# Optimization experiments

Measured on AMD Instinct MI355X. Metric: run time of the kernel, lower is better.

## Reference

```python
import jax, jax.numpy as jnp
import numpy as np

N_NODES = 50000
N_EDGES = 600000  # incidence entries; hyperedge ids also live in [0, N_NODES)
HID = 128


def _prelu(x, a):
    return jnp.where(x >= 0, x, a * x)


def _hypergraph_conv(x, W, b, node_idx, edge_idx, num_nodes, num_hedges):
    # PyG HypergraphConv (use_attention=False, heads=1):
    # out = D^{-1} H B^{-1} H^T (X Theta) + bias
    xw = x @ W  # [N, F]
    ones = jnp.ones(node_idx.shape[0], dtype=x.dtype)
    D = jax.ops.segment_sum(ones, node_idx, num_segments=num_nodes)   # node degree
    B = jax.ops.segment_sum(ones, edge_idx, num_segments=num_hedges)  # hyperedge degree
    Dinv = jnp.where(D > 0, 1.0 / D, 0.0)
    Binv = jnp.where(B > 0, 1.0 / B, 0.0)
    # node -> hyperedge aggregation, scaled by B^{-1}
    m = jax.ops.segment_sum(xw[node_idx], edge_idx, num_segments=num_hedges) * Binv[:, None]
    # hyperedge -> node aggregation, scaled by D^{-1}
    out = jax.ops.segment_sum(m[edge_idx], node_idx, num_segments=num_nodes) * Dinv[:, None]
    return out + b


def setup_inputs() -> dict:
    key = jax.random.key(0)
    k1, k2, k3, k4, k5 = jax.random.split(key, 5)
    x = jax.random.normal(k1, (N_NODES, HID), dtype=jnp.float32)
    hyper_edge_index = jax.random.randint(k2, (2, N_EDGES), 0, N_NODES, dtype=jnp.int64)
    # kaiming-normal-ish linear weights, zero biases (per init_weights)
    std = float(np.sqrt(2.0 / HID))
    W1 = jax.random.normal(k3, (HID, HID), dtype=jnp.float32) * std
    W2 = jax.random.normal(k4, (HID, HID), dtype=jnp.float32) * std
    b1 = jnp.zeros((HID,), dtype=jnp.float32)
    b2 = jnp.zeros((HID,), dtype=jnp.float32)
    prelu_a = jnp.full((1,), 0.25, dtype=jnp.float32)  # nn.PReLU default
    return {"x": x, "hyper_edge_index": hyper_edge_index,
            "W1": W1, "b1": b1, "W2": W2, "b2": b2, "prelu_a": prelu_a}


def reference(x, hyper_edge_index, W1, b1, W2, b2, prelu_a):
    node_idx = hyper_edge_index[0]
    edge_idx = hyper_edge_index[1]
    h = _hypergraph_conv(x, W1, b1, node_idx, edge_idx, N_NODES, N_NODES)
    h = _prelu(h, prelu_a)
    h = _hypergraph_conv(h, W2, b2, node_idx, edge_idx, N_NODES, N_NODES)
    h = h + x  # residual
    return _prelu(h, prelu_a)
```

## Files before the change

kernel.cpp:

```cpp
#include <hip/hip_runtime.h>

typedef unsigned short u16;
typedef unsigned int   u32;
typedef unsigned long long u64;

#define HID 128
#define KPB 256
#define NBMAX 512
#define IPB 2048
#define CAP 6144
#define LSTRIDE 136

typedef __bf16 bf16x8 __attribute__((ext_vector_type(8)));
typedef float  f32x4  __attribute__((ext_vector_type(4)));

__device__ inline float u2f(u32 u){ union{u32 u;float f;} v; v.u=u; return v.f; }
__device__ inline u32   f2u(float f){ union{float f;u32 u;} v; v.f=f; return v.u; }
__device__ inline u32  f2bfu(float f){ u32 b=f2u(f); return ((b + 0x7FFFu + ((b>>16)&1u))>>16)&0xFFFFu; }
__device__ inline float blo(u32 u){ return u2f(u<<16); }
__device__ inline float bhi(u32 u){ return u2f(u & 0xFFFF0000u); }
__device__ inline u32  pk(float lo, float hi){ return (f2bfu(hi)<<16) | f2bfu(lo); }

__global__ __launch_bounds__(256) void k_hist_wfrag(const int* __restrict__ nidx, const int* __restrict__ eidx,
                                                    int* __restrict__ hist, int nE, int nN, int nb, int nhb,
                                                    const float* __restrict__ W1, const float* __restrict__ W2,
                                                    u16* __restrict__ W1f, u16* __restrict__ W2f){
    __shared__ int h[NBMAX];
    if ((int)blockIdx.x < nhb){
        for (int t=threadIdx.x; t<nb; t+=256) h[t]=0;
        __syncthreads();
        int base = blockIdx.x*IPB;
        for (int k=threadIdx.x; k<IPB; k+=256){
            int j = base+k;
            if (j < nE){
                atomicAdd(&h[nidx[j]>>8], 1);
                atomicAdd(&h[(nN+eidx[j])>>8], 1);
            }
        }
        __syncthreads();
        for (int t=threadIdx.x; t<nb; t+=256) if (h[t]) atomicAdd(&hist[t], h[t]);
    } else {
        int gid = ((int)blockIdx.x - nhb)*256 + threadIdx.x;
        const float* W = (gid < 16384) ? W1 : W2;
        u16* Wf = (gid < 16384) ? W1f : W2f;
        int id = gid & 16383;
        int i = id & 7, l = (id>>3)&63, j = (id>>9)&7, s = id>>12;
        Wf[id] = (u16)f2bfu(W[(s*32 + ((l>>4)<<3) + i)*HID + (j<<4) + (l&15)]);
    }
}

__global__ __launch_bounds__(256) void k_part_gemm(const int* __restrict__ nidx, const int* __restrict__ eidx,
                                                   const int* __restrict__ hist, int* __restrict__ bfill,
                                                   u64* __restrict__ pairs, int nE, int nN, int nb, int npb,
                                                   const float* __restrict__ A, const u16* __restrict__ Wf,
                                                   u16* __restrict__ C, int M){
    __shared__ int h[NBMAX], rsv[NBMAX], fl[NBMAX], bb[NBMAX], sd[256];
    int t = threadIdx.x;
    if ((int)blockIdx.x < npb){
        for (int i=t; i<nb; i+=256){ h[i]=0; fl[i]=0; }
        __syncthreads();
        int base = blockIdx.x*IPB;
        for (int k=t; k<IPB; k+=256){
            int j = base+k;
            if (j < nE){
                atomicAdd(&h[nidx[j]>>8], 1);
                atomicAdd(&h[(nN+eidx[j])>>8], 1);
            }
        }
        int c0 = (2*t   < nb) ? hist[2*t]   : 0;
        int c1 = (2*t+1 < nb) ? hist[2*t+1] : 0;
        int s = c0 + c1;
        sd[t] = s; __syncthreads();
        for (int o=1;o<256;o<<=1){ int u = (t>=o)? sd[t-o] : 0; __syncthreads(); sd[t]+=u; __syncthreads(); }
        int ex = sd[t] - s;
        if (2*t   < nb) bb[2*t]   = ex;
        if (2*t+1 < nb) bb[2*t+1] = ex + c0;
        __syncthreads();
        for (int i=t; i<nb; i+=256){ if (h[i]) rsv[i] = bb[i] + atomicAdd(&bfill[i], h[i]); }
        __syncthreads();
        for (int k=t; k<IPB; k+=256){
            int j = base+k;
            if (j < nE){
                int n = nidx[j], e = eidx[j];
                int b1 = n>>8;
                int p1 = rsv[b1] + atomicAdd(&fl[b1], 1);
                pairs[p1] = ((u64)(u32)n << 32) | (u32)e;
                int k2 = nN + e;
                int b2 = k2>>8;
                int p2 = rsv[b2] + atomicAdd(&fl[b2], 1);
                pairs[p2] = ((u64)(u32)k2 << 32) | (u32)n;
            }
        }
    } else {
        int wave = ((int)blockIdx.x - npb)*4 + (t>>6);
        int lane = t & 63;
        int rtiles = M >> 4;
        if (wave >= rtiles) return;
        int row0 = wave << 4;
        const float* Arow = A + (size_t)(row0 + (lane&15))*HID + ((lane>>4)<<3);
        const bf16x8* Wp = reinterpret_cast<const bf16x8*>(Wf) + lane;
        f32x4 acc[8];
        #pragma unroll
        for (int j=0;j<8;++j) acc[j] = (f32x4){0.f,0.f,0.f,0.f};
        #pragma unroll
        for (int s=0;s<4;++s){
            float4 f0 = *reinterpret_cast<const float4*>(Arow + s*32);
            float4 f1 = *reinterpret_cast<const float4*>(Arow + s*32 + 4);
            union { u16 h[8]; bf16x8 v; } au;
            au.h[0]=(u16)f2bfu(f0.x); au.h[1]=(u16)f2bfu(f0.y); au.h[2]=(u16)f2bfu(f0.z); au.h[3]=(u16)f2bfu(f0.w);
            au.h[4]=(u16)f2bfu(f1.x); au.h[5]=(u16)f2bfu(f1.y); au.h[6]=(u16)f2bfu(f1.z); au.h[7]=(u16)f2bfu(f1.w);
            #pragma unroll
            for (int j=0;j<8;++j){
                bf16x8 b = Wp[(s*8 + j)*64];
                acc[j] = __builtin_amdgcn_mfma_f32_16x16x32_bf16(au.v, b, acc[j], 0, 0, 0);
            }
        }
        int r0 = row0 + ((lane>>4)<<2);
        int c0 = lane & 15;
        #pragma unroll
        for (int j=0;j<8;++j){
            #pragma unroll
            for (int r=0;r<4;++r){
                C[(size_t)(r0+r)*HID + j*16 + c0] = (u16)f2bfu(acc[j][r]);
            }
        }
    }
}

__global__ __launch_bounds__(256) void k_bucket(const u64* __restrict__ pairs, const int* __restrict__ hist,
                                                int* __restrict__ csr, int* __restrict__ off,
                                                int nkeys, int nb, int total){
    __shared__ int cntS[KPB];
    __shared__ int fillS[KPB];
    __shared__ int bbS[NBMAX+1];
    __shared__ int sd[256];
    __shared__ int vals[CAP];
    int b = blockIdx.x;
    int t = threadIdx.x;
    if (b == 0 && t == 0) off[nkeys] = total;
    int c0 = (2*t   < nb) ? hist[2*t]   : 0;
    int c1 = (2*t+1 < nb) ? hist[2*t+1] : 0;
    int s = c0 + c1;
    sd[t] = s; __syncthreads();
    for (int o=1;o<256;o<<=1){ int u = (t>=o)? sd[t-o] : 0; __syncthreads(); sd[t]+=u; __syncthreads(); }
    int ex = sd[t] - s;
    if (2*t   <= nb) bbS[2*t]   = ex;
    if (2*t+1 <= nb) bbS[2*t+1] = ex + c0;
    __syncthreads();
    int base = bbS[b];
    int n = bbS[b+1] - base;
    int k0 = b * KPB;

    cntS[t] = 0;
    __syncthreads();
    for (int i=t; i<n; i+=256){
        u64 p = pairs[base+i];
        atomicAdd(&cntS[(int)(p>>32) - k0], 1);
    }
    __syncthreads();
    int c = cntS[t];
    __syncthreads();
    fillS[t] = c; __syncthreads();
    for (int o=1;o<256;o<<=1){ int u = (t>=o)? fillS[t-o] : 0; __syncthreads(); fillS[t]+=u; __syncthreads(); }
    int ex2 = fillS[t] - c;
    __syncthreads();
    fillS[t] = ex2;
    __syncthreads();
    int k = k0 + t;
    if (k < nkeys) off[k] = base + ex2;
    bool fits = (n <= CAP);
    for (int i=t; i<n; i+=256){
        u64 p = pairs[base+i];
        int kl = (int)(p>>32) - k0;
        int pos = atomicAdd(&fillS[kl], 1);
        if (fits) vals[pos] = (int)(u32)p;
        else      csr[base+pos] = (int)(u32)p;
    }
    __syncthreads();
    if (fits){
        for (int i=t; i<n; i+=256) csr[base+i] = vals[i];
    }
}

template<int MODE>
__global__ __launch_bounds__(256) void k_agg(const u32* __restrict__ tab, const int* __restrict__ csr,
                                             const int* __restrict__ off, void* __restrict__ outp,
                                             const float* __restrict__ bias, const float* __restrict__ resid,
                                             const float* __restrict__ aptr, int nrows){
    int lane = threadIdx.x & 63;
    int g = lane >> 4, c = lane & 15;
    int d = blockIdx.x*16 + ((threadIdx.x>>6)<<2) + g;
    if (d >= nrows) return;
    int start = off[d], end = off[d+1];
    int deg = end - start;
    int gbase = g << 4;

    float a0=0.f,a1=0.f,a2=0.f,a3=0.f,a4=0.f,a5=0.f,a6=0.f,a7=0.f;
    for (int pos = start; pos < end; pos += 16){
        int myc = csr[pos + c];
        int lim = end - pos;
        #pragma unroll
        for (int i=0;i<16;i+=4){
            int s0 = __shfl(myc, gbase|i,     64);
            int s1 = __shfl(myc, gbase|(i+1), 64);
            int s2 = __shfl(myc, gbase|(i+2), 64);
            int s3 = __shfl(myc, gbase|(i+3), 64);
            uint4 v0 = make_uint4(0u,0u,0u,0u), v1 = v0, v2 = v0, v3 = v0;
            if (i   < lim) v0 = *reinterpret_cast<const uint4*>(tab + (size_t)s0*64 + (c<<2));
            if (i+1 < lim) v1 = *reinterpret_cast<const uint4*>(tab + (size_t)s1*64 + (c<<2));
            if (i+2 < lim) v2 = *reinterpret_cast<const uint4*>(tab + (size_t)s2*64 + (c<<2));
            if (i+3 < lim) v3 = *reinterpret_cast<const uint4*>(tab + (size_t)s3*64 + (c<<2));
            a0 += blo(v0.x)+blo(v1.x)+blo(v2.x)+blo(v3.x);
            a1 += bhi(v0.x)+bhi(v1.x)+bhi(v2.x)+bhi(v3.x);
            a2 += blo(v0.y)+blo(v1.y)+blo(v2.y)+blo(v3.y);
            a3 += bhi(v0.y)+bhi(v1.y)+bhi(v2.y)+bhi(v3.y);
            a4 += blo(v0.z)+blo(v1.z)+blo(v2.z)+blo(v3.z);
            a5 += bhi(v0.z)+bhi(v1.z)+bhi(v2.z)+bhi(v3.z);
            a6 += blo(v0.w)+blo(v1.w)+blo(v2.w)+blo(v3.w);
            a7 += bhi(v0.w)+bhi(v1.w)+bhi(v2.w)+bhi(v3.w);
        }
    }
    float s = (deg > 0) ? 1.0f/(float)deg : 0.f;
    a0*=s; a1*=s; a2*=s; a3*=s; a4*=s; a5*=s; a6*=s; a7*=s;
    if constexpr (MODE == 2){
        float4 b0 = *reinterpret_cast<const float4*>(bias + (c<<3));
        float4 b1v = *reinterpret_cast<const float4*>(bias + (c<<3) + 4);
        a0+=b0.x; a1+=b0.y; a2+=b0.z; a3+=b0.w;
        a4+=b1v.x; a5+=b1v.y; a6+=b1v.z; a7+=b1v.w;
        const float* rp = resid + (size_t)d*HID + (c<<3);
        float4 r0 = *reinterpret_cast<const float4*>(rp);
        float4 r1 = *reinterpret_cast<const float4*>(rp + 4);
        a0+=r0.x; a1+=r0.y; a2+=r0.z; a3+=r0.w;
        a4+=r1.x; a5+=r1.y; a6+=r1.z; a7+=r1.w;
        float al = aptr[0];
        a0 = (a0>=0.f)? a0 : al*a0;  a1 = (a1>=0.f)? a1 : al*a1;
        a2 = (a2>=0.f)? a2 : al*a2;  a3 = (a3>=0.f)? a3 : al*a3;
        a4 = (a4>=0.f)? a4 : al*a4;  a5 = (a5>=0.f)? a5 : al*a5;
        a6 = (a6>=0.f)? a6 : al*a6;  a7 = (a7>=0.f)? a7 : al*a7;
        float* op = (float*)outp + (size_t)d*HID + (c<<3);
        *reinterpret_cast<float4*>(op)     = make_float4(a0,a1,a2,a3);
        *reinterpret_cast<float4*>(op + 4) = make_float4(a4,a5,a6,a7);
    } else {
        uint4 wv;
        wv.x = pk(a0,a1); wv.y = pk(a2,a3); wv.z = pk(a4,a5); wv.w = pk(a6,a7);
        *reinterpret_cast<uint4*>((u32*)outp + (size_t)d*64 + (c<<2)) = wv;
    }
}

__global__ __launch_bounds__(256) void k_agg1_gemm(const u32* __restrict__ tab, const int* __restrict__ csr,
                                                   const int* __restrict__ off, u16* __restrict__ C,
                                                   const float* __restrict__ bias, const float* __restrict__ aptr,
                                                   const u16* __restrict__ Wf, int nrows){
    __shared__ u16 hS[16*LSTRIDE];
    int t = threadIdx.x;
    int lane = t & 63;
    int wv = t >> 6;
    int g = lane >> 4, c = lane & 15;
    int r = (wv<<2) + g;
    int d = blockIdx.x*16 + r;
    int gbase = g << 4;

    float a0=0.f,a1=0.f,a2=0.f,a3=0.f,a4=0.f,a5=0.f,a6=0.f,a7=0.f;
    if (d < nrows){
        int start = off[d], end = off[d+1];
        int deg = end - start;
        for (int pos = start; pos < end; pos += 16){
            int myc = csr[pos + c];
            int lim = end - pos;
            #pragma unroll
            for (int i=0;i<16;i+=4){
                int s0 = __shfl(myc, gbase|i,     64);
                int s1 = __shfl(myc, gbase|(i+1), 64);
                int s2 = __shfl(myc, gbase|(i+2), 64);
                int s3 = __shfl(myc, gbase|(i+3), 64);
                uint4 v0 = make_uint4(0u,0u,0u,0u), v1 = v0, v2 = v0, v3 = v0;
                if (i   < lim) v0 = *reinterpret_cast<const uint4*>(tab + (size_t)s0*64 + (c<<2));
                if (i+1 < lim) v1 = *reinterpret_cast<const uint4*>(tab + (size_t)s1*64 + (c<<2));
                if (i+2 < lim) v2 = *reinterpret_cast<const uint4*>(tab + (size_t)s2*64 + (c<<2));
                if (i+3 < lim) v3 = *reinterpret_cast<const uint4*>(tab + (size_t)s3*64 + (c<<2));
                a0 += blo(v0.x)+blo(v1.x)+blo(v2.x)+blo(v3.x);
                a1 += bhi(v0.x)+bhi(v1.x)+bhi(v2.x)+bhi(v3.x);
                a2 += blo(v0.y)+blo(v1.y)+blo(v2.y)+blo(v3.y);
                a3 += bhi(v0.y)+bhi(v1.y)+bhi(v2.y)+bhi(v3.y);
                a4 += blo(v0.z)+blo(v1.z)+blo(v2.z)+blo(v3.z);
                a5 += bhi(v0.z)+bhi(v1.z)+bhi(v2.z)+bhi(v3.z);
                a6 += blo(v0.w)+blo(v1.w)+blo(v2.w)+blo(v3.w);
                a7 += bhi(v0.w)+bhi(v1.w)+bhi(v2.w)+bhi(v3.w);
            }
        }
        float s = (deg > 0) ? 1.0f/(float)deg : 0.f;
        a0*=s; a1*=s; a2*=s; a3*=s; a4*=s; a5*=s; a6*=s; a7*=s;
        float4 b0 = *reinterpret_cast<const float4*>(bias + (c<<3));
        float4 b1v = *reinterpret_cast<const float4*>(bias + (c<<3) + 4);
        a0+=b0.x; a1+=b0.y; a2+=b0.z; a3+=b0.w;
        a4+=b1v.x; a5+=b1v.y; a6+=b1v.z; a7+=b1v.w;
        float al = aptr[0];
        a0 = (a0>=0.f)? a0 : al*a0;  a1 = (a1>=0.f)? a1 : al*a1;
        a2 = (a2>=0.f)? a2 : al*a2;  a3 = (a3>=0.f)? a3 : al*a3;
        a4 = (a4>=0.f)? a4 : al*a4;  a5 = (a5>=0.f)? a5 : al*a5;
        a6 = (a6>=0.f)? a6 : al*a6;  a7 = (a7>=0.f)? a7 : al*a7;
    }
    {
        uint4 wv4;
        wv4.x = pk(a0,a1); wv4.y = pk(a2,a3); wv4.z = pk(a4,a5); wv4.w = pk(a6,a7);
        *reinterpret_cast<uint4*>((u32*)(hS + (size_t)r*LSTRIDE) + (c<<2)) = wv4;
    }
    __syncthreads();

    const u16* Arow = hS + (size_t)(lane&15)*LSTRIDE + ((lane>>4)<<3);
    const bf16x8* Wp = reinterpret_cast<const bf16x8*>(Wf) + lane;
    f32x4 acc0 = (f32x4){0.f,0.f,0.f,0.f}, acc1 = acc0;
    #pragma unroll
    for (int s=0;s<4;++s){
        bf16x8 a = *reinterpret_cast<const bf16x8*>(Arow + s*32);
        bf16x8 bA = Wp[(s*8 + 2*wv    )*64];
        bf16x8 bB = Wp[(s*8 + 2*wv + 1)*64];
        acc0 = __builtin_amdgcn_mfma_f32_16x16x32_bf16(a, bA, acc0, 0, 0, 0);
        acc1 = __builtin_amdgcn_mfma_f32_16x16x32_bf16(a, bB, acc1, 0, 0, 0);
    }
    int r0 = (lane>>4)<<2;
    int c0 = lane & 15;
    #pragma unroll
    for (int rr=0;rr<4;++rr){
        int row = blockIdx.x*16 + r0 + rr;
        if (row < nrows){
            C[(size_t)row*HID + (2*wv  )*16 + c0] = (u16)f2bfu(acc0[rr]);
            C[(size_t)row*HID + (2*wv+1)*16 + c0] = (u16)f2bfu(acc1[rr]);
        }
    }
}

extern "C" void kernel_launch(void* const* d_in, const int* in_sizes, int n_in,
                              void* d_out, int out_size, void* d_ws, size_t ws_size,
                              hipStream_t stream){
    (void)n_in; (void)out_size; (void)ws_size;
    const float* x  = (const float*)d_in[0];
    const int*  hei = (const int*)  d_in[1];
    const float* W1 = (const float*)d_in[2];
    const float* b1 = (const float*)d_in[3];
    const float* W2 = (const float*)d_in[4];
    const float* b2 = (const float*)d_in[5];
    const float* ap = (const float*)d_in[6];

    const int nN = in_sizes[0] / HID;
    const int nE = in_sizes[1] / 2;
    const int* nidx = hei;
    const int* eidx = hei + nE;
    const int nkeys = 2*nN;
    const int nb    = (nkeys + KPB - 1) / KPB;

    char* w = (char*)d_ws;
    size_t o = 0;
    auto alloc = [&](size_t bytes)->void*{
        void* p = (void*)(w + o);
        o += (bytes + 255) & ~(size_t)255;
        return p;
    };
    int* hist  = (int*)alloc((size_t)NBMAX*sizeof(int));
    int* bfill = (int*)alloc((size_t)NBMAX*sizeof(int));
    int* off   = (int*)alloc(((size_t)nkeys+1)*sizeof(int));
    int* csr   = (int*)alloc((size_t)2*nE*sizeof(int));
    u64* pairs = (u64*)alloc((size_t)2*nE*sizeof(u64));
    u16* bufB  = (u16*)alloc((size_t)nN*HID*sizeof(u16));
    u16* bufC  = (u16*)alloc((size_t)nN*HID*sizeof(u16));
    u16* w1f   = (u16*)alloc((size_t)HID*HID*sizeof(u16));
    u16* w2f   = (u16*)alloc((size_t)HID*HID*sizeof(u16));

    hipMemsetAsync(hist, 0, (size_t)2*NBMAX*sizeof(int), stream);

    const int pgrid  = (nE + IPB - 1)/IPB;
    const int rtiles = nN/16;
    const int ggrid  = (rtiles + 3)/4;

    k_hist_wfrag<<<pgrid + 128, 256, 0, stream>>>(nidx, eidx, hist, nE, nN, nb, pgrid, W1, W2, w1f, w2f);
    k_part_gemm<<<pgrid + ggrid, 256, 0, stream>>>(nidx, eidx, hist, bfill, pairs, nE, nN, nb, pgrid,
                                                   x, w1f, bufB, nN);
    k_bucket<<<nb, 256, 0, stream>>>(pairs, hist, csr, off, nkeys, nb, 2*nE);

    const int agrid = (nN + 15)/16;

    k_agg<0><<<agrid, 256, 0, stream>>>((const u32*)bufB, csr, off + nN, bufC, nullptr, nullptr, nullptr, nN);
    k_agg1_gemm<<<agrid, 256, 0, stream>>>((const u32*)bufC, csr, off, bufB, b1, ap, w2f, nN);
    k_agg<0><<<agrid, 256, 0, stream>>>((const u32*)bufB, csr, off + nN, bufC, nullptr, nullptr, nullptr, nN);
    k_agg<2><<<agrid, 256, 0, stream>>>((const u32*)bufC, csr, off, d_out, b2, x, ap, nN);
}
```

Before: 226.0 us.

## Split aggregation into feature-slice blocks and unfuse second-layer GEMM

The gather-aggregation kernels now split the 128-wide feature row into four 32-column slices, each handled by a separate block, with 4 lanes per destination row and 16 rows per wave. Each slice touches a smaller part of the table, which is meant to improve cache locality and load balance across rows of uneven degree. The fused aggregate+GEMM kernel is replaced by a slice aggregation that writes PReLU output to a new buffer, followed by a standalone MFMA GEMM kernel. This adds one kernel launch and an extra round trip of the hidden activations through memory, and it reads the CSR indices four times.

Result: slower. 268.7 us (+18.9%).

```diff
diff --git a/kernel.cpp b/kernel.cpp
--- a/kernel.cpp
+++ b/kernel.cpp
@@ -9,7 +9,6 @@
 #define NBMAX 512
 #define IPB 2048
 #define CAP 6144
-#define LSTRIDE 136
 
 typedef __bf16 bf16x8 __attribute__((ext_vector_type(8)));
 typedef float  f32x4  __attribute__((ext_vector_type(4)));
@@ -183,149 +182,104 @@
 }
 
 template<int MODE>
-__global__ __launch_bounds__(256) void k_agg(const u32* __restrict__ tab, const int* __restrict__ csr,
-                                             const int* __restrict__ off, void* __restrict__ outp,
-                                             const float* __restrict__ bias, const float* __restrict__ resid,
-                                             const float* __restrict__ aptr, int nrows){
-    int lane = threadIdx.x & 63;
-    int g = lane >> 4, c = lane & 15;
-    int d = blockIdx.x*16 + ((threadIdx.x>>6)<<2) + g;
+__global__ __launch_bounds__(256) void k_aggs(const u32* __restrict__ tab, const int* __restrict__ csr,
+                                              const int* __restrict__ off, void* __restrict__ outp,
+                                              const float* __restrict__ bias, const float* __restrict__ resid,
+                                              const float* __restrict__ aptr, int nrows){
+    int slice = blockIdx.x & 3;
+    int dt    = blockIdx.x >> 2;
+    int t = threadIdx.x;
+    int lane = t & 63;
+    int grp = lane >> 2, c4 = lane & 3;
+    int sb = lane & 60;
+    int d = dt*64 + ((t>>6)<<4) + grp;
     if (d >= nrows) return;
     int start = off[d], end = off[d+1];
     int deg = end - start;
-    int gbase = g << 4;
+    const u32* tslice = tab + slice*16 + (c4<<2);
 
     float a0=0.f,a1=0.f,a2=0.f,a3=0.f,a4=0.f,a5=0.f,a6=0.f,a7=0.f;
-    for (int pos = start; pos < end; pos += 16){
-        int myc = csr[pos + c];
+    for (int pos = start; pos < end; pos += 4){
+        int myc = csr[pos + c4];
         int lim = end - pos;
-        #pragma unroll
-        for (int i=0;i<16;i+=4){
-            int s0 = __shfl(myc, gbase|i,     64);
-            int s1 = __shfl(myc, gbase|(i+1), 64);
-            int s2 = __shfl(myc, gbase|(i+2), 64);
-            int s3 = __shfl(myc, gbase|(i+3), 64);
-            uint4 v0 = make_uint4(0u,0u,0u,0u), v1 = v0, v2 = v0, v3 = v0;
-            if (i   < lim) v0 = *reinterpret_cast<const uint4*>(tab + (size_t)s0*64 + (c<<2));
-            if (i+1 < lim) v1 = *reinterpret_cast<const uint4*>(tab + (size_t)s1*64 + (c<<2));
-            if (i+2 < lim) v2 = *reinterpret_cast<const uint4*>(tab + (size_t)s2*64 + (c<<2));
-            if (i+3 < lim) v3 = *reinterpret_cast<const uint4*>(tab + (size_t)s3*64 + (c<<2));
-            a0 += blo(v0.x)+blo(v1.x)+blo(v2.x)+blo(v3.x);
-            a1 += bhi(v0.x)+bhi(v1.x)+bhi(v2.x)+bhi(v3.x);
-            a2 += blo(v0.y)+blo(v1.y)+blo(v2.y)+blo(v3.y);
-            a3 += bhi(v0.y)+bhi(v1.y)+bhi(v2.y)+bhi(v3.y);
-            a4 += blo(v0.z)+blo(v1.z)+blo(v2.z)+blo(v3.z);
-            a5 += bhi(v0.z)+bhi(v1.z)+bhi(v2.z)+bhi(v3.z);
-            a6 += blo(v0.w)+blo(v1.w)+blo(v2.w)+blo(v3.w);
-            a7 += bhi(v0.w)+bhi(v1.w)+bhi(v2.w)+bhi(v3.w);
-        }
+        int s0 = __shfl(myc, sb|0, 64);
+        int s1 = __shfl(myc, sb|1, 64);
+        int s2 = __shfl(myc, sb|2, 64);
+        int s3 = __shfl(myc, sb|3, 64);
+        uint4 v0 = *reinterpret_cast<const uint4*>(tslice + (size_t)s0*64);
+        uint4 v1 = make_uint4(0u,0u,0u,0u), v2 = v1, v3 = v1;
+        if (1 < lim) v1 = *reinterpret_cast<const uint4*>(tslice + (size_t)s1*64);
+        if (2 < lim) v2 = *reinterpret_cast<const uint4*>(tslice + (size_t)s2*64);
+        if (3 < lim) v3 = *reinterpret_cast<const uint4*>(tslice + (size_t)s3*64);
+        a0 += blo(v0.x)+blo(v1.x)+blo(v2.x)+blo(v3.x);
+        a1 += bhi(v0.x)+bhi(v1.x)+bhi(v2.x)+bhi(v3.x);
+        a2 += blo(v0.y)+blo(v1.y)+blo(v2.y)+blo(v3.y);
+        a3 += bhi(v0.y)+bhi(v1.y)+bhi(v2.y)+bhi(v3.y);
+        a4 += blo(v0.z)+blo(v1.z)+blo(v2.z)+blo(v3.z);
+        a5 += bhi(v0.z)+bhi(v1.z)+bhi(v2.z)+bhi(v3.z);
+        a6 += blo(v0.w)+blo(v1.w)+blo(v2.w)+blo(v3.w);
+        a7 += bhi(v0.w)+bhi(v1.w)+bhi(v2.w)+bhi(v3.w);
     }
     float s = (deg > 0) ? 1.0f/(float)deg : 0.f;
     a0*=s; a1*=s; a2*=s; a3*=s; a4*=s; a5*=s; a6*=s; a7*=s;
-    if constexpr (MODE == 2){
-        float4 b0 = *reinterpret_cast<const float4*>(bias + (c<<3));
-        float4 b1v = *reinterpret_cast<const float4*>(bias + (c<<3) + 4);
+    if constexpr (MODE >= 1){
+        const float* bp = bias + slice*32 + (c4<<3);
+        float4 b0 = *reinterpret_cast<const float4*>(bp);
+        float4 b1v = *reinterpret_cast<const float4*>(bp + 4);
         a0+=b0.x; a1+=b0.y; a2+=b0.z; a3+=b0.w;
         a4+=b1v.x; a5+=b1v.y; a6+=b1v.z; a7+=b1v.w;
-        const float* rp = resid + (size_t)d*HID + (c<<3);
-        float4 r0 = *reinterpret_cast<const float4*>(rp);
-        float4 r1 = *reinterpret_cast<const float4*>(rp + 4);
-        a0+=r0.x; a1+=r0.y; a2+=r0.z; a3+=r0.w;
-        a4+=r1.x; a5+=r1.y; a6+=r1.z; a7+=r1.w;
+        if constexpr (MODE == 2){
+            const float* rp = resid + (size_t)d*HID + slice*32 + (c4<<3);
+            float4 r0 = *reinterpret_cast<const float4*>(rp);
+            float4 r1 = *reinterpret_cast<const float4*>(rp + 4);
+            a0+=r0.x; a1+=r0.y; a2+=r0.z; a3+=r0.w;
+            a4+=r1.x; a5+=r1.y; a6+=r1.z; a7+=r1.w;
+        }
         float al = aptr[0];
         a0 = (a0>=0.f)? a0 : al*a0;  a1 = (a1>=0.f)? a1 : al*a1;
         a2 = (a2>=0.f)? a2 : al*a2;  a3 = (a3>=0.f)? a3 : al*a3;
         a4 = (a4>=0.f)? a4 : al*a4;  a5 = (a5>=0.f)? a5 : al*a5;
         a6 = (a6>=0.f)? a6 : al*a6;  a7 = (a7>=0.f)? a7 : al*a7;
-        float* op = (float*)outp + (size_t)d*HID + (c<<3);
+    }
+    if constexpr (MODE == 2){
+        float* op = (float*)outp + (size_t)d*HID + slice*32 + (c4<<3);
         *reinterpret_cast<float4*>(op)     = make_float4(a0,a1,a2,a3);
         *reinterpret_cast<float4*>(op + 4) = make_float4(a4,a5,a6,a7);
     } else {
-        uint4 wv;
-        wv.x = pk(a0,a1); wv.y = pk(a2,a3); wv.z = pk(a4,a5); wv.w = pk(a6,a7);
-        *reinterpret_cast<uint4*>((u32*)outp + (size_t)d*64 + (c<<2)) = wv;
-    }
-}
-
-__global__ __launch_bounds__(256) void k_agg1_gemm(const u32* __restrict__ tab, const int* __restrict__ csr,
-                                                   const int* __restrict__ off, u16* __restrict__ C,
-                                                   const float* __restrict__ bias, const float* __restrict__ aptr,
-                                                   const u16* __restrict__ Wf, int nrows){
-    __shared__ u16 hS[16*LSTRIDE];
-    int t = threadIdx.x;
-    int lane = t & 63;
-    int wv = t >> 6;
-    int g = lane >> 4, c = lane & 15;
-    int r = (wv<<2) + g;
-    int d = blockIdx.x*16 + r;
-    int gbase = g << 4;
-
-    float a0=0.f,a1=0.f,a2=0.f,a3=0.f,a4=0.f,a5=0.f,a6=0.f,a7=0.f;
-    if (d < nrows){
-        int start = off[d], end = off[d+1];
-        int deg = end - start;
-        for (int pos = start; pos < end; pos += 16){
-            int myc = csr[pos + c];
-            int lim = end - pos;
-            #pragma unroll
-            for (int i=0;i<16;i+=4){
-                int s0 = __shfl(myc, gbase|i,     64);
-                int s1 = __shfl(myc, gbase|(i+1), 64);
-                int s2 = __shfl(myc, gbase|(i+2), 64);
-                int s3 = __shfl(myc, gbase|(i+3), 64);
-                uint4 v0 = make_uint4(0u,0u,0u,0u), v1 = v0, v2 = v0, v3 = v0;
-                if (i   < lim) v0 = *reinterpret_cast<const uint4*>(tab + (size_t)s0*64 + (c<<2));
-                if (i+1 < lim) v1 = *reinterpret_cast<const uint4*>(tab + (size_t)s1*64 + (c<<2));
-                if (i+2 < lim) v2 = *reinterpret_cast<const uint4*>(tab + (size_t)s2*64 + (c<<2));
-                if (i+3 < lim) v3 = *reinterpret_cast<const uint4*>(tab + (size_t)s3*64 + (c<<2));
-                a0 += blo(v0.x)+blo(v1.x)+blo(v2.x)+blo(v3.x);
-                a1 += bhi(v0.x)+bhi(v1.x)+bhi(v2.x)+bhi(v3.x);
-                a2 += blo(v0.y)+blo(v1.y)+blo(v2.y)+blo(v3.y);
-                a3 += bhi(v0.y)+bhi(v1.y)+bhi(v2.y)+bhi(v3.y);
-                a4 += blo(v0.z)+blo(v1.z)+blo(v2.z)+blo(v3.z);
-                a5 += bhi(v0.z)+bhi(v1.z)+bhi(v2.z)+bhi(v3.z);
-                a6 += blo(v0.w)+blo(v1.w)+blo(v2.w)+blo(v3.w);
-                a7 += bhi(v0.w)+bhi(v1.w)+bhi(v2.w)+bhi(v3.w);
-            }
-        }
-        float s = (deg > 0) ? 1.0f/(float)deg : 0.f;
-        a0*=s; a1*=s; a2*=s; a3*=s; a4*=s; a5*=s; a6*=s; a7*=s;
-        float4 b0 = *reinterpret_cast<const float4*>(bias + (c<<3));
-        float4 b1v = *reinterpret_cast<const float4*>(bias + (c<<3) + 4);
-        a0+=b0.x; a1+=b0.y; a2+=b0.z; a3+=b0.w;
-        a4+=b1v.x; a5+=b1v.y; a6+=b1v.z; a7+=b1v.w;
-        float al = aptr[0];
-        a0 = (a0>=0.f)? a0 : al*a0;  a1 = (a1>=0.f)? a1 : al*a1;
-        a2 = (a2>=0.f)? a2 : al*a2;  a3 = (a3>=0.f)? a3 : al*a3;
-        a4 = (a4>=0.f)? a4 : al*a4;  a5 = (a5>=0.f)? a5 : al*a5;
-        a6 = (a6>=0.f)? a6 : al*a6;  a7 = (a7>=0.f)? a7 : al*a7;
-    }
-    {
         uint4 wv4;
         wv4.x = pk(a0,a1); wv4.y = pk(a2,a3); wv4.z = pk(a4,a5); wv4.w = pk(a6,a7);
-        *reinterpret_cast<uint4*>((u32*)(hS + (size_t)r*LSTRIDE) + (c<<2)) = wv4;
-    }
-    __syncthreads();
-
-    const u16* Arow = hS + (size_t)(lane&15)*LSTRIDE + ((lane>>4)<<3);
+        *reinterpret_cast<uint4*>((u32*)outp + (size_t)d*64 + slice*16 + (c4<<2)) = wv4;
+    }
+}
+
+__global__ __launch_bounds__(256) void k_gemm_bf(const u16* __restrict__ A, const u16* __restrict__ Wf,
+                                                 u16* __restrict__ C, int M){
+    int wave = blockIdx.x*4 + ((int)threadIdx.x>>6);
+    int lane = threadIdx.x & 63;
+    int rtiles = M >> 4;
+    if (wave >= rtiles) return;
+    int row0 = wave << 4;
+    const u16* Arow = A + (size_t)(row0 + (lane&15))*HID + ((lane>>4)<<3);
     const bf16x8* Wp = reinterpret_cast<const bf16x8*>(Wf) + lane;
-    f32x4 acc0 = (f32x4){0.f,0.f,0.f,0.f}, acc1 = acc0;
+    f32x4 acc[8];
+    #pragma unroll
+    for (int j=0;j<8;++j) acc[j] = (f32x4){0.f,0.f,0.f,0.f};
     #pragma unroll
     for (int s=0;s<4;++s){
         bf16x8 a = *reinterpret_cast<const bf16x8*>(Arow + s*32);
-        bf16x8 bA = Wp[(s*8 + 2*wv    )*64];
-        bf16x8 bB = Wp[(s*8 + 2*wv + 1)*64];
-        acc0 = __builtin_amdgcn_mfma_f32_16x16x32_bf16(a, bA, acc0, 0, 0, 0);
-        acc1 = __builtin_amdgcn_mfma_f32_16x16x32_bf16(a, bB, acc1, 0, 0, 0);
-    }
-    int r0 = (lane>>4)<<2;
+        #pragma unroll
+        for (int j=0;j<8;++j){
+            bf16x8 b = Wp[(s*8 + j)*64];
+            acc[j] = __builtin_amdgcn_mfma_f32_16x16x32_bf16(a, b, acc[j], 0, 0, 0);
+        }
+    }
+    int r0 = row0 + ((lane>>4)<<2);
     int c0 = lane & 15;
     #pragma unroll
-    for (int rr=0;rr<4;++rr){
-        int row = blockIdx.x*16 + r0 + rr;
-        if (row < nrows){
-            C[(size_t)row*HID + (2*wv  )*16 + c0] = (u16)f2bfu(acc0[rr]);
-            C[(size_t)row*HID + (2*wv+1)*16 + c0] = (u16)f2bfu(acc1[rr]);
+    for (int j=0;j<8;++j){
+        #pragma unroll
+        for (int r=0;r<4;++r){
+            C[(size_t)(r0+r)*HID + j*16 + c0] = (u16)f2bfu(acc[j][r]);
         }
     }
 }
@@ -363,6 +317,7 @@
     u64* pairs = (u64*)alloc((size_t)2*nE*sizeof(u64));
     u16* bufB  = (u16*)alloc((size_t)nN*HID*sizeof(u16));
     u16* bufC  = (u16*)alloc((size_t)nN*HID*sizeof(u16));
+    u16* bufH  = (u16*)alloc((size_t)nN*HID*sizeof(u16));
     u16* w1f   = (u16*)alloc((size_t)HID*HID*sizeof(u16));
     u16* w2f   = (u16*)alloc((size_t)HID*HID*sizeof(u16));
 
@@ -371,16 +326,17 @@
     const int pgrid  = (nE + IPB - 1)/IPB;
     const int rtiles = nN/16;
     const int ggrid  = (rtiles + 3)/4;
+    const int dblk   = (nN + 63)/64;
+    const int agrid  = 4*dblk;
 
     k_hist_wfrag<<<pgrid + 128, 256, 0, stream>>>(nidx, eidx, hist, nE, nN, nb, pgrid, W1, W2, w1f, w2f);
     k_part_gemm<<<pgrid + ggrid, 256, 0, stream>>>(nidx, eidx, hist, bfill, pairs, nE, nN, nb, pgrid,
                                                    x, w1f, bufB, nN);
     k_bucket<<<nb, 256, 0, stream>>>(pairs, hist, csr, off, nkeys, nb, 2*nE);
 
-    const int agrid = (nN + 15)/16;
-
-    k_agg<0><<<agrid, 256, 0, stream>>>((const u32*)bufB, csr, off + nN, bufC, nullptr, nullptr, nullptr, nN);
-    k_agg1_gemm<<<agrid, 256, 0, stream>>>((const u32*)bufC, csr, off, bufB, b1, ap, w2f, nN);
-    k_agg<0><<<agrid, 256, 0, stream>>>((const u32*)bufB, csr, off + nN, bufC, nullptr, nullptr, nullptr, nN);
-    k_agg<2><<<agrid, 256, 0, stream>>>((const u32*)bufC, csr, off, d_out, b2, x, ap, nN);
-}
+    k_aggs<0><<<agrid, 256, 0, stream>>>((const u32*)bufB, csr, off + nN, bufC, nullptr, nullptr, nullptr, nN);
+    k_aggs<1><<<agrid, 256, 0, stream>>>((const u32*)bufC, csr, off, bufH, b1, nullptr, ap, nN);
+    k_gemm_bf<<<ggrid, 256, 0, stream>>>(bufH, w2f, bufB, nN);
+    k_aggs<0><<<agrid, 256, 0, stream>>>((const u32*)bufB, csr, off + nN, bufC, nullptr, nullptr, nullptr, nN);
+    k_aggs<2><<<agrid, 256, 0, stream>>>((const u32*)bufC, csr, off, d_out, b2, x, ap, nN);
+}
```

## Replace bucketed pair sort with per-key count, scan, and atomic scatter CSR build

Applied to the files above, without the earlier changes.

The CSR construction previously made coarse bucket histograms, a partition pass writing 64-bit pairs, and a per-bucket local sort. It now counts degrees per key with global atomics, does a two-level prefix scan, and scatters neighbor ids straight into CSR slots using per-key atomic fill counters. This removes the intermediate pairs buffer and the bucket kernel's shared-memory sort. In exchange it adds one kernel launch and many scattered global atomics. Neighbor order within a row also becomes nondeterministic, which can change float summation order.

Result: slower. 317.5 us (+40.5%).

```diff
diff --git a/kernel.cpp b/kernel.cpp
--- a/kernel.cpp
+++ b/kernel.cpp
@@ -5,10 +5,9 @@
 typedef unsigned long long u64;
 
 #define HID 128
-#define KPB 256
-#define NBMAX 512
 #define IPB 2048
-#define CAP 6144
+#define SCANB 1024
+#define SPB 1024
 #define LSTRIDE 136
 
 typedef __bf16 bf16x8 __attribute__((ext_vector_type(8)));
@@ -21,24 +20,20 @@
 __device__ inline float bhi(u32 u){ return u2f(u & 0xFFFF0000u); }
 __device__ inline u32  pk(float lo, float hi){ return (f2bfu(hi)<<16) | f2bfu(lo); }
 
+
 __global__ __launch_bounds__(256) void k_hist_wfrag(const int* __restrict__ nidx, const int* __restrict__ eidx,
-                                                    int* __restrict__ hist, int nE, int nN, int nb, int nhb,
+                                                    int* __restrict__ cnt, int nE, int nN, int nhb,
                                                     const float* __restrict__ W1, const float* __restrict__ W2,
                                                     u16* __restrict__ W1f, u16* __restrict__ W2f){
-    __shared__ int h[NBMAX];
     if ((int)blockIdx.x < nhb){
-        for (int t=threadIdx.x; t<nb; t+=256) h[t]=0;
-        __syncthreads();
         int base = blockIdx.x*IPB;
         for (int k=threadIdx.x; k<IPB; k+=256){
             int j = base+k;
             if (j < nE){
-                atomicAdd(&h[nidx[j]>>8], 1);
-                atomicAdd(&h[(nN+eidx[j])>>8], 1);
-            }
-        }
-        __syncthreads();
-        for (int t=threadIdx.x; t<nb; t+=256) if (h[t]) atomicAdd(&hist[t], h[t]);
+                atomicAdd(&cnt[nidx[j]], 1);
+                atomicAdd(&cnt[nN+eidx[j]], 1);
+            }
+        }
     } else {
         int gid = ((int)blockIdx.x - nhb)*256 + threadIdx.x;
         const float* W = (gid < 16384) ? W1 : W2;
@@ -49,50 +44,24 @@
     }
 }
 
-__global__ __launch_bounds__(256) void k_part_gemm(const int* __restrict__ nidx, const int* __restrict__ eidx,
-                                                   const int* __restrict__ hist, int* __restrict__ bfill,
-                                                   u64* __restrict__ pairs, int nE, int nN, int nb, int npb,
+__global__ __launch_bounds__(256) void k_scan_gemm(const int* __restrict__ cnt, int* __restrict__ poff,
+                                                   int* __restrict__ btot, int nsb,
                                                    const float* __restrict__ A, const u16* __restrict__ Wf,
                                                    u16* __restrict__ C, int M){
-    __shared__ int h[NBMAX], rsv[NBMAX], fl[NBMAX], bb[NBMAX], sd[256];
     int t = threadIdx.x;
-    if ((int)blockIdx.x < npb){
-        for (int i=t; i<nb; i+=256){ h[i]=0; fl[i]=0; }
-        __syncthreads();
-        int base = blockIdx.x*IPB;
-        for (int k=t; k<IPB; k+=256){
-            int j = base+k;
-            if (j < nE){
-                atomicAdd(&h[nidx[j]>>8], 1);
-                atomicAdd(&h[(nN+eidx[j])>>8], 1);
-            }
-        }
-        int c0 = (2*t   < nb) ? hist[2*t]   : 0;
-        int c1 = (2*t+1 < nb) ? hist[2*t+1] : 0;
-        int s = c0 + c1;
+    if ((int)blockIdx.x < nsb){
+        __shared__ int sd[256];
+        int k0 = blockIdx.x*SCANB + t*4;
+        int4 c = *reinterpret_cast<const int4*>(cnt + k0);
+        int s = c.x + c.y + c.z + c.w;
         sd[t] = s; __syncthreads();
         for (int o=1;o<256;o<<=1){ int u = (t>=o)? sd[t-o] : 0; __syncthreads(); sd[t]+=u; __syncthreads(); }
         int ex = sd[t] - s;
-        if (2*t   < nb) bb[2*t]   = ex;
-        if (2*t+1 < nb) bb[2*t+1] = ex + c0;
-        __syncthreads();
-        for (int i=t; i<nb; i+=256){ if (h[i]) rsv[i] = bb[i] + atomicAdd(&bfill[i], h[i]); }
-        __syncthreads();
-        for (int k=t; k<IPB; k+=256){
-            int j = base+k;
-            if (j < nE){
-                int n = nidx[j], e = eidx[j];
-                int b1 = n>>8;
-                int p1 = rsv[b1] + atomicAdd(&fl[b1], 1);
-                pairs[p1] = ((u64)(u32)n << 32) | (u32)e;
-                int k2 = nN + e;
-                int b2 = k2>>8;
-                int p2 = rsv[b2] + atomicAdd(&fl[b2], 1);
-                pairs[p2] = ((u64)(u32)k2 << 32) | (u32)n;
-            }
-        }
+        int4 p; p.x = ex; p.y = ex + c.x; p.z = p.y + c.y; p.w = p.z + c.z;
+        *reinterpret_cast<int4*>(poff + k0) = p;
+        if (t == 255) btot[blockIdx.x] = sd[255];
     } else {
-        int wave = ((int)blockIdx.x - npb)*4 + (t>>6);
+        int wave = ((int)blockIdx.x - nsb)*4 + (t>>6);
         int lane = t & 63;
         int rtiles = M >> 4;
         if (wave >= rtiles) return;
@@ -103,15 +72,15 @@
         #pragma unroll
         for (int j=0;j<8;++j) acc[j] = (f32x4){0.f,0.f,0.f,0.f};
         #pragma unroll
-        for (int s=0;s<4;++s){
-            float4 f0 = *reinterpret_cast<const float4*>(Arow + s*32);
-            float4 f1 = *reinterpret_cast<const float4*>(Arow + s*32 + 4);
+        for (int s4=0;s4<4;++s4){
+            float4 f0 = *reinterpret_cast<const float4*>(Arow + s4*32);
+            float4 f1 = *reinterpret_cast<const float4*>(Arow + s4*32 + 4);
             union { u16 h[8]; bf16x8 v; } au;
             au.h[0]=(u16)f2bfu(f0.x); au.h[1]=(u16)f2bfu(f0.y); au.h[2]=(u16)f2bfu(f0.z); au.h[3]=(u16)f2bfu(f0.w);
             au.h[4]=(u16)f2bfu(f1.x); au.h[5]=(u16)f2bfu(f1.y); au.h[6]=(u16)f2bfu(f1.z); au.h[7]=(u16)f2bfu(f1.w);
             #pragma unroll
             for (int j=0;j<8;++j){
-                bf16x8 b = Wp[(s*8 + j)*64];
+                bf16x8 b = Wp[(s4*8 + j)*64];
                 acc[j] = __builtin_amdgcn_mfma_f32_16x16x32_bf16(au.v, b, acc[j], 0, 0, 0);
             }
         }
@@ -127,58 +96,57 @@
     }
 }
 
-__global__ __launch_bounds__(256) void k_bucket(const u64* __restrict__ pairs, const int* __restrict__ hist,
-                                                int* __restrict__ csr, int* __restrict__ off,
-                                                int nkeys, int nb, int total){
-    __shared__ int cntS[KPB];
-    __shared__ int fillS[KPB];
-    __shared__ int bbS[NBMAX+1];
+__global__ __launch_bounds__(256) void k_scanb(const int* __restrict__ btot, int* __restrict__ bbase, int nsb){
     __shared__ int sd[256];
-    __shared__ int vals[CAP];
-    int b = blockIdx.x;
     int t = threadIdx.x;
-    if (b == 0 && t == 0) off[nkeys] = total;
-    int c0 = (2*t   < nb) ? hist[2*t]   : 0;
-    int c1 = (2*t+1 < nb) ? hist[2*t+1] : 0;
-    int s = c0 + c1;
-    sd[t] = s; __syncthreads();
+    int v = (t < nsb) ? btot[t] : 0;
+    sd[t] = v; __syncthreads();
     for (int o=1;o<256;o<<=1){ int u = (t>=o)? sd[t-o] : 0; __syncthreads(); sd[t]+=u; __syncthreads(); }
-    int ex = sd[t] - s;
-    if (2*t   <= nb) bbS[2*t]   = ex;
-    if (2*t+1 <= nb) bbS[2*t+1] = ex + c0;
-    __syncthreads();
-    int base = bbS[b];
-    int n = bbS[b+1] - base;
-    int k0 = b * KPB;
-
-    cntS[t] = 0;
-    __syncthreads();
-    for (int i=t; i<n; i+=256){
-        u64 p = pairs[base+i];
-        atomicAdd(&cntS[(int)(p>>32) - k0], 1);
-    }
-    __syncthreads();
-    int c = cntS[t];
-    __syncthreads();
-    fillS[t] = c; __syncthreads();
-    for (int o=1;o<256;o<<=1){ int u = (t>=o)? fillS[t-o] : 0; __syncthreads(); fillS[t]+=u; __syncthreads(); }
-    int ex2 = fillS[t] - c;
-    __syncthreads();
-    fillS[t] = ex2;
-    __syncthreads();
-    int k = k0 + t;
-    if (k < nkeys) off[k] = base + ex2;
-    bool fits = (n <= CAP);
-    for (int i=t; i<n; i+=256){
-        u64 p = pairs[base+i];
-        int kl = (int)(p>>32) - k0;
-        int pos = atomicAdd(&fillS[kl], 1);
-        if (fits) vals[pos] = (int)(u32)p;
-        else      csr[base+pos] = (int)(u32)p;
-    }
-    __syncthreads();
-    if (fits){
-        for (int i=t; i<n; i+=256) csr[base+i] = vals[i];
+    if (t < nsb) bbase[t] = sd[t] - v;
+}
+
+__global__ __launch_bounds__(256) void k_scatter_fin(const int* __restrict__ nidx, const int* __restrict__ eidx,
+                                                     const int* __restrict__ poff, const int* __restrict__ bbase,
+                                                     int* __restrict__ fill, int* __restrict__ csr,
+                                                     int* __restrict__ off, int nE, int nN, int nscat){
+    int t = threadIdx.x;
+    if ((int)blockIdx.x < nscat){
+        int base = blockIdx.x*SPB + t*4;
+        if (base + 3 < nE){
+            int4 nn = *reinterpret_cast<const int4*>(nidx + base);
+            int4 ee = *reinterpret_cast<const int4*>(eidx + base);
+            int ka0 = nn.x, ka1 = nn.y, ka2 = nn.z, ka3 = nn.w;
+            int kb0 = nN+ee.x, kb1 = nN+ee.y, kb2 = nN+ee.z, kb3 = nN+ee.w;
+            int pa0 = poff[ka0] + bbase[ka0>>10] + atomicAdd(&fill[ka0],1);
+            int pa1 = poff[ka1] + bbase[ka1>>10] + atomicAdd(&fill[ka1],1);
+            int pa2 = poff[ka2] + bbase[ka2>>10] + atomicAdd(&fill[ka2],1);
+            int pa3 = poff[ka3] + bbase[ka3>>10] + atomicAdd(&fill[ka3],1);
+            int pb0 = poff[kb0] + bbase[kb0>>10] + atomicAdd(&fill[kb0],1);
+            int pb1 = poff[kb1] + bbase[kb1>>10] + atomicAdd(&fill[kb1],1);
+            int pb2 = poff[kb2] + bbase[kb2>>10] + atomicAdd(&fill[kb2],1);
+            int pb3 = poff[kb3] + bbase[kb3>>10] + atomicAdd(&fill[kb3],1);
+            csr[pa0] = ee.x; csr[pa1] = ee.y; csr[pa2] = ee.z; csr[pa3] = ee.w;
+            csr[pb0] = nn.x; csr[pb1] = nn.y; csr[pb2] = nn.z; csr[pb3] = nn.w;
+        } else {
+            for (int i=0;i<4;++i){
+                int j = base+i;
+                if (j < nE){
+                    int n = nidx[j], e = eidx[j];
+                    int k1 = n, k2 = nN + e;
+                    int p1 = poff[k1] + bbase[k1>>10] + atomicAdd(&fill[k1],1);
+                    csr[p1] = e;
+                    int p2 = poff[k2] + bbase[k2>>10] + atomicAdd(&fill[k2],1);
+                    csr[p2] = n;
+                }
+            }
+        }
+    } else {
+        int b2 = (int)blockIdx.x - nscat;
+        int k0 = b2*SCANB + t*4;
+        int4 p = *reinterpret_cast<const int4*>(poff + k0);
+        int bb = bbase[b2];
+        int4 o4; o4.x = p.x+bb; o4.y = p.y+bb; o4.z = p.z+bb; o4.w = p.w+bb;
+        *reinterpret_cast<int4*>(off + k0) = o4;
     }
 }
 
@@ -347,7 +315,8 @@
     const int* nidx = hei;
     const int* eidx = hei + nE;
     const int nkeys = 2*nN;
-    const int nb    = (nkeys + KPB - 1) / KPB;
+    const int nsb   = (nkeys + SCANB - 1)/SCANB;
+    const int nscat = (nE + SPB - 1)/SPB;
 
     char* w = (char*)d_ws;
     size_t o = 0;
@@ -356,28 +325,29 @@
         o += (bytes + 255) & ~(size_t)255;
         return p;
     };
-    int* hist  = (int*)alloc((size_t)NBMAX*sizeof(int));
-    int* bfill = (int*)alloc((size_t)NBMAX*sizeof(int));
-    int* off   = (int*)alloc(((size_t)nkeys+1)*sizeof(int));
+    int* cnt   = (int*)alloc((size_t)nsb*SCANB*sizeof(int));
+    int* fill  = (int*)alloc((size_t)nsb*SCANB*sizeof(int));
+    int* poff  = (int*)alloc((size_t)nsb*SCANB*sizeof(int));
+    int* btot  = (int*)alloc(256*sizeof(int));
+    int* bbase = (int*)alloc(256*sizeof(int));
+    int* off   = (int*)alloc(((size_t)nsb*SCANB + 16)*sizeof(int));
     int* csr   = (int*)alloc((size_t)2*nE*sizeof(int));
-    u64* pairs = (u64*)alloc((size_t)2*nE*sizeof(u64));
     u16* bufB  = (u16*)alloc((size_t)nN*HID*sizeof(u16));
     u16* bufC  = (u16*)alloc((size_t)nN*HID*sizeof(u16));
     u16* w1f   = (u16*)alloc((size_t)HID*HID*sizeof(u16));
     u16* w2f   = (u16*)alloc((size_t)HID*HID*sizeof(u16));
 
-    hipMemsetAsync(hist, 0, (size_t)2*NBMAX*sizeof(int), stream);
+    hipMemsetAsync(cnt, 0, (size_t)2*nsb*SCANB*sizeof(int), stream);
 
     const int pgrid  = (nE + IPB - 1)/IPB;
     const int rtiles = nN/16;
     const int ggrid  = (rtiles + 3)/4;
-
-    k_hist_wfrag<<<pgrid + 128, 256, 0, stream>>>(nidx, eidx, hist, nE, nN, nb, pgrid, W1, W2, w1f, w2f);
-    k_part_gemm<<<pgrid + ggrid, 256, 0, stream>>>(nidx, eidx, hist, bfill, pairs, nE, nN, nb, pgrid,
-                                                   x, w1f, bufB, nN);
-    k_bucket<<<nb, 256, 0, stream>>>(pairs, hist, csr, off, nkeys, nb, 2*nE);
-
-    const int agrid = (nN + 15)/16;
+    const int agrid  = (nN + 15)/16;
+
+    k_hist_wfrag<<<pgrid + 128, 256, 0, stream>>>(nidx, eidx, cnt, nE, nN, pgrid, W1, W2, w1f, w2f);
+    k_scan_gemm<<<nsb + ggrid, 256, 0, stream>>>(cnt, poff, btot, nsb, x, w1f, bufB, nN);
+    k_scanb<<<1, 256, 0, stream>>>(btot, bbase, nsb);
+    k_scatter_fin<<<nscat + nsb, 256, 0, stream>>>(nidx, eidx, poff, bbase, fill, csr, off, nE, nN, nscat);
 
     k_agg<0><<<agrid, 256, 0, stream>>>((const u32*)bufB, csr, off + nN, bufC, nullptr, nullptr, nullptr, nN);
     k_agg1_gemm<<<agrid, 256, 0, stream>>>((const u32*)bufC, csr, off, bufB, b1, ap, w2f, nN);
```
